# Optimization experiments

Hardware: AMD Instinct MI355X
Metric: run time of the kernel (lower is better)

The kernel has to match this reference:

```python
import jax, jax.numpy as jnp
import numpy as np

B, S, D = 4, 2048, 1024
H = 16
HD = D // H  # 64


def setup_inputs() -> dict:
    key = jax.random.key(0)
    ks = jax.random.split(key, 4)
    scale = 0.02
    return {
        "hidden_states": jax.random.normal(ks[0], (B, S, D), dtype=jnp.float32),
        "attention_mask": jnp.zeros((B, 1, 1, S), dtype=jnp.float32),
        "Wq": jax.random.normal(ks[1], (D, D), dtype=jnp.float32) * scale,
        "bq": jnp.zeros((D,), dtype=jnp.float32),
        "Wk": jax.random.normal(ks[2], (D, D), dtype=jnp.float32) * scale,
        "bk": jnp.zeros((D,), dtype=jnp.float32),
        "Wv": jax.random.normal(ks[3], (D, D), dtype=jnp.float32) * scale,
        "bv": jnp.zeros((D,), dtype=jnp.float32),
    }


def reference(hidden_states, attention_mask, Wq, bq, Wk, bk, Wv, bv):
    # linear projections: x @ W^T + b (torch nn.Linear convention); here W stored as [D,D]
    def proj(x, W, b):
        y = jnp.einsum("bsd,ed->bse", x, W) + b
        # [B,S,D] -> [B,H,S,HD]
        return y.reshape(B, S, H, HD).transpose(0, 2, 1, 3)

    q = proj(hidden_states, Wq, bq)
    k = proj(hidden_states, Wk, bk)
    v = proj(hidden_states, Wv, bv)

    scores = jnp.einsum("bhqd,bhkd->bhqk", q, k) / jnp.sqrt(jnp.float32(HD))
    scores = scores + attention_mask  # additive mask broadcast [B,1,1,S]
    probs = jax.nn.softmax(scores, axis=-1)  # dropout p=0 -> identity
    ctx = jnp.einsum("bhqk,bhkd->bhqd", probs, v)
    ctx = ctx.transpose(0, 2, 1, 3).reshape(B, S, D)
    return ctx
```

## Files before the change

### kernel.cpp

```cpp
#include <hip/hip_runtime.h>
#include <hip/hip_bf16.h>

typedef __attribute__((ext_vector_type(4))) float f32x4;
typedef __attribute__((ext_vector_type(16))) float f32x16;
typedef __attribute__((ext_vector_type(8))) short bf16x8;
typedef __attribute__((ext_vector_type(4))) unsigned int u32x4;
typedef unsigned short u16;

#define DEV static __device__ __forceinline__

DEV u16 f2bf(float f) {
    union { float f; unsigned int u; } v; v.f = f;
    unsigned int r = v.u + 0x7FFFu + ((v.u >> 16) & 1u);
    return (u16)(r >> 16);
}

DEV unsigned int cvt_pk(float lo, float hi) {
    unsigned int r;
    asm("v_cvt_pk_bf16_f32 %0, %1, %2" : "=v"(r) : "v"(lo), "v"(hi));
    return r;
}

DEV void pswap(unsigned int& a, unsigned int& b) {
    asm volatile("v_permlane32_swap_b32 %0, %1" : "+v"(a), "+v"(b));
}

DEV void async16(const void* g, void* l) {
    __builtin_amdgcn_global_load_lds((const __attribute__((address_space(1))) unsigned int*)g,
                                     (__attribute__((address_space(3))) unsigned int*)l, 16, 0, 0);
}

__global__ void cvt_all(const float4* __restrict__ x, const float4* __restrict__ wq,
                        const float4* __restrict__ wk, const float4* __restrict__ wv,
                        ushort4* __restrict__ xb, ushort4* __restrict__ wb,
                        const float* __restrict__ mask, float* __restrict__ em) {
    int bid = blockIdx.x;
    if (bid >= 11264) {
        int i = (bid - 11264) * 256 + threadIdx.x;
        em[i] = __builtin_amdgcn_exp2f(mask[i] * 1.44269504088896340736f);
        return;
    }
    const float4* s;
    ushort4* d;
    int i;
    if (bid < 8192) {
        s = x; d = xb; i = bid * 256 + threadIdx.x;
    } else {
        int r = bid - 8192;
        int wsel = r >> 10;
        s = (wsel == 0) ? wq : (wsel == 1) ? wk : wv;
        d = wb + (size_t)wsel * 262144;
        i = (r & 1023) * 256 + threadIdx.x;
    }
    float4 v = s[i];
    ushort4 o;
    o.x = f2bf(v.x); o.y = f2bf(v.y); o.z = f2bf(v.z); o.w = f2bf(v.w);
    d[i] = o;
}

__launch_bounds__(256, 2)
__global__ void qkv_gemm(const u16* __restrict__ xb, const u16* __restrict__ wb,
                         const float* __restrict__ bq, const float* __restrict__ bk,
                         const float* __restrict__ bv, const float* __restrict__ em,
                         u16* __restrict__ Qb, u16* __restrict__ Kb, u16* __restrict__ Vtb) {
    __shared__ u16 Al[2][128 * 64];
    __shared__ u16 Bl[2][128 * 64];
    const int t = threadIdx.x, ln = t & 63, w = t >> 6;
    const int wr = w >> 1, wc = w & 1;
    const int m0 = blockIdx.x * 128, e0 = blockIdx.y * 128, p = blockIdx.z;
    const u16* Wp = wb + (size_t)p * 1048576;
    const float* bias = (p == 0) ? bq : (p == 1) ? bk : bv;

    const int srow = t >> 3, scol = (t & 7) * 8;

    f32x4 acc[4][4];
#pragma unroll
    for (int i = 0; i < 4; i++)
#pragma unroll
        for (int j = 0; j < 4; j++) acc[i][j] = (f32x4){0.f, 0.f, 0.f, 0.f};

#define G_STAGE(buf, kk)                                                              \
    {                                                                                 \
        _Pragma("unroll")                                                             \
        for (int c = 0; c < 4; c++) {                                                 \
            int r = c * 32 + srow;                                                    \
            async16(&xb[(size_t)(m0 + r) * 1024 + (kk) + scol], &Al[buf][r * 64 + scol]); \
            async16(&Wp[(size_t)(e0 + r) * 1024 + (kk) + scol], &Bl[buf][r * 64 + scol]); \
        }                                                                             \
    }

    G_STAGE(0, 0);
    __syncthreads();
    int cur = 0;
    for (int kt = 0; kt < 16; kt++) {
        if (kt < 15) G_STAGE(cur ^ 1, (kt + 1) * 64);
#pragma unroll
        for (int kc = 0; kc < 2; kc++) {
            bf16x8 a[4], bb[4];
#pragma unroll
            for (int mf = 0; mf < 4; mf++)
                a[mf] = *(const bf16x8*)&Al[cur][(wr * 64 + mf * 16 + (ln & 15)) * 64 + kc * 32 + (ln >> 4) * 8];
#pragma unroll
            for (int nf = 0; nf < 4; nf++)
                bb[nf] = *(const bf16x8*)&Bl[cur][(wc * 64 + nf * 16 + (ln & 15)) * 64 + kc * 32 + (ln >> 4) * 8];
            __builtin_amdgcn_s_setprio(1);
#pragma unroll
            for (int mf = 0; mf < 4; mf++)
#pragma unroll
                for (int nf = 0; nf < 4; nf++)
                    acc[mf][nf] = __builtin_amdgcn_mfma_f32_16x16x32_bf16(a[mf], bb[nf], acc[mf][nf], 0, 0, 0);
            __builtin_amdgcn_s_setprio(0);
        }
        __syncthreads();
        cur ^= 1;
    }
#undef G_STAGE

    const int q16 = ln & 15, g = ln >> 4;
    if (p == 2) {
#pragma unroll
        for (int nf = 0; nf < 4; nf++) {
            int e = e0 + wc * 64 + nf * 16 + q16;
            float bias_v = bias[e];
            int h = e >> 6, hd = e & 63;
#pragma unroll
            for (int mf = 0; mf < 4; mf++) {
                int m = m0 + wr * 64 + mf * 16 + g * 4;
                int b = m >> 11, s = m & 2047;
                f32x4 emv = *(const f32x4*)&em[b * 2048 + s];
                ushort4 pk;
                pk.x = f2bf((acc[mf][nf][0] + bias_v) * emv[0]);
                pk.y = f2bf((acc[mf][nf][1] + bias_v) * emv[1]);
                pk.z = f2bf((acc[mf][nf][2] + bias_v) * emv[2]);
                pk.w = f2bf((acc[mf][nf][3] + bias_v) * emv[3]);
                *(ushort4*)&Vtb[((size_t)((b * 16 + h) * 64 + hd)) * 2048 + s] = pk;
            }
        }
    } else {
        const float qscale = (p == 0) ? 0.18033688011112042f : 1.0f;
        u16* out = (p == 0) ? Qb : Kb;
#pragma unroll
        for (int nf = 0; nf < 4; nf++) {
            int e = e0 + wc * 64 + nf * 16 + q16;
            float bias_v = bias[e];
            int h = e >> 6, hd = e & 63;
#pragma unroll
            for (int mf = 0; mf < 4; mf++) {
#pragma unroll
                for (int r = 0; r < 4; r++) {
                    int m = m0 + wr * 64 + mf * 16 + g * 4 + r;
                    int b = m >> 11, s = m & 2047;
                    out[((size_t)(b * 16 + h) * 2048 + s) * 64 + hd] = f2bf((acc[mf][nf][r] + bias_v) * qscale);
                }
            }
        }
    }
}

__launch_bounds__(128, 3)
__global__ void attn_kernel(const u16* __restrict__ Q, const u16* __restrict__ K,
                            const u16* __restrict__ Vt, const float* __restrict__ em,
                            float* __restrict__ out) {
    __shared__ u16 Kl[64 * 64];
    __shared__ u16 Vl[64 * 64];
    const int t = threadIdx.x, ln = t & 63, w = t >> 6;
    const int ln31 = ln & 31, hi = ln >> 5, ln7 = ln & 7;

    const int bid0 = blockIdx.x;
    const int swz = (bid0 & 7) * 256 + (bid0 >> 3);
    const int qbi = swz & 31, bh = swz >> 5;
    const int b = bh >> 4, h = bh & 15;
    const int qr = qbi * 64 + w * 32;
    const size_t base = (size_t)bh * 2048 * 64;

    bf16x8 aq[4];
#pragma unroll
    for (int ds = 0; ds < 4; ds++)
        aq[ds] = *(const bf16x8*)&Q[base + (size_t)(qr + ln31) * 64 + ds * 16 + hi * 8];

    const int rbase = t >> 3;
    const int sc = (t & 7) ^ (rbase & 7);

#define A_STAGE(kk)                                                                        \
    {                                                                                      \
        _Pragma("unroll")                                                                  \
        for (int i = 0; i < 4; i++) {                                                      \
            int row = i * 16 + rbase;                                                      \
            async16(&K[base + (size_t)((kk) + row) * 64 + sc * 8], &Kl[(i * 128 + t) * 8]); \
            async16(&Vt[base + (size_t)row * 2048 + (kk) + sc * 8], &Vl[(i * 128 + t) * 8]); \
        }                                                                                  \
    }

    f32x16 accT[2];
    accT[0] = (f32x16){};
    accT[1] = (f32x16){};
    f32x4 lacc = (f32x4){0.f, 0.f, 0.f, 0.f};

    for (int kt = 0; kt < 32; kt++) {
        const int k0 = kt * 64;
        if (kt) __syncthreads();
        A_STAGE(k0);
        __syncthreads();

#pragma unroll
        for (int kti = 0; kti < 2; kti++) {
            bf16x8 ka[4];
#pragma unroll
            for (int ds = 0; ds < 4; ds++)
                ka[ds] = *(const bf16x8*)&Kl[(kti * 32 + ln31) * 64 + (((ds << 1) | hi) ^ ln7) * 8];

            f32x4 em4[4];
#pragma unroll
            for (int rf = 0; rf < 4; rf++)
                em4[rf] = *(const f32x4*)&em[b * 2048 + k0 + kti * 32 + rf * 8 + hi * 4];

            f32x16 z = (f32x16){};
            __builtin_amdgcn_s_setprio(1);
#pragma unroll
            for (int ds = 0; ds < 4; ds++)
                z = __builtin_amdgcn_mfma_f32_32x32x16_bf16(ka[ds], aq[ds], z, 0, 0, 0);
            __builtin_amdgcn_s_setprio(0);

            float p[16];
#pragma unroll
            for (int i = 0; i < 16; i++) p[i] = __builtin_amdgcn_exp2f(z[i]);

#pragma unroll
            for (int rf = 0; rf < 4; rf++) {
                lacc[0] += p[4 * rf + 0] * em4[rf][0];
                lacc[1] += p[4 * rf + 1] * em4[rf][1];
                lacc[2] += p[4 * rf + 2] * em4[rf][2];
                lacc[3] += p[4 * rf + 3] * em4[rf][3];
            }

            unsigned int pk00 = cvt_pk(p[0], p[1]),   pk01 = cvt_pk(p[2], p[3]);
            unsigned int pk10 = cvt_pk(p[4], p[5]),   pk11 = cvt_pk(p[6], p[7]);
            unsigned int pk20 = cvt_pk(p[8], p[9]),   pk21 = cvt_pk(p[10], p[11]);
            unsigned int pk30 = cvt_pk(p[12], p[13]), pk31 = cvt_pk(p[14], p[15]);
            pswap(pk00, pk10); pswap(pk01, pk11);
            pswap(pk20, pk30); pswap(pk21, pk31);
            u32x4 pb[2];
            pb[0][0] = pk00; pb[0][1] = pk01; pb[0][2] = pk10; pb[0][3] = pk11;
            pb[1][0] = pk20; pb[1][1] = pk21; pb[1][2] = pk30; pb[1][3] = pk31;

            __builtin_amdgcn_s_setprio(1);
#pragma unroll
            for (int s = 0; s < 2; s++) {
                bf16x8 pv = *(const bf16x8*)&pb[s];
#pragma unroll
                for (int dt = 0; dt < 2; dt++) {
                    bf16x8 va = *(const bf16x8*)&Vl[(dt * 32 + ln31) * 64 +
                                                    ((kti * 4 + s * 2 + hi) ^ ln7) * 8];
                    accT[dt] = __builtin_amdgcn_mfma_f32_32x32x16_bf16(va, pv, accT[dt], 0, 0, 0);
                }
            }
            __builtin_amdgcn_s_setprio(0);
        }
    }
#undef A_STAGE

    float l = (lacc[0] + lacc[1]) + (lacc[2] + lacc[3]);
    l += __shfl_xor(l, 32);
    float inv = 1.0f / l;
    int q = qr + ln31;
#pragma unroll
    for (int dt = 0; dt < 2; dt++) {
#pragma unroll
        for (int rf = 0; rf < 4; rf++) {
            f32x4 o;
            o[0] = accT[dt][4 * rf + 0] * inv;
            o[1] = accT[dt][4 * rf + 1] * inv;
            o[2] = accT[dt][4 * rf + 2] * inv;
            o[3] = accT[dt][4 * rf + 3] * inv;
            *(f32x4*)&out[((size_t)(b * 2048 + q)) * 1024 + h * 64 + dt * 32 + rf * 8 + hi * 4] = o;
        }
    }
}

extern "C" void kernel_launch(void* const* d_in, const int* in_sizes, int n_in,
                              void* d_out, int out_size, void* d_ws, size_t ws_size,
                              hipStream_t stream) {
    const float* x    = (const float*)d_in[0];
    const float* mask = (const float*)d_in[1];
    const float* Wq   = (const float*)d_in[2];
    const float* bq   = (const float*)d_in[3];
    const float* Wk   = (const float*)d_in[4];
    const float* bk   = (const float*)d_in[5];
    const float* Wv   = (const float*)d_in[6];
    const float* bv   = (const float*)d_in[7];
    float* out = (float*)d_out;

    char* ws = (char*)d_ws;
    if (ws_size < (size_t)73433088) return;
    u16* xb   = (u16*)(ws);
    u16* wb   = (u16*)(ws + 16777216);
    u16* Qb   = (u16*)(ws + 23068672);
    u16* Kb   = (u16*)(ws + 39845888);
    u16* Vtb  = (u16*)(ws + 56623104);
    float* em = (float*)(ws + 73400320);

    cvt_all<<<11296, 256, 0, stream>>>((const float4*)x, (const float4*)Wq, (const float4*)Wk,
                                       (const float4*)Wv, (ushort4*)xb, (ushort4*)wb, mask, em);
    qkv_gemm<<<dim3(64, 8, 3), 256, 0, stream>>>(xb, wb, bq, bk, bv, em, Qb, Kb, Vtb);
    attn_kernel<<<2048, 128, 0, stream>>>(Qb, Kb, Vtb, em, out);
}
```

Baseline: 196.5 us.

## Double-buffer K/V tiles with 4-wave blocks and stage mask in LDS

The attention kernel moves from 2-wave blocks covering 64 query rows to 4-wave blocks covering 128 rows, so each K/V tile staged in shared memory serves twice as many waves. K/V staging is now double-buffered: the next tile is prefetched asynchronously while the current one is consumed, which removes one barrier per iteration and overlaps loads with MFMA work. The per-batch mask vector is copied once into LDS rather than read from global memory every step. The cost is more LDS per block (about 40KB), which may limit how many blocks fit per CU, and the grid halves to 1024 blocks.

After: 170.7 us. 13.2% less time.

```diff
diff --git a/kernel.cpp b/kernel.cpp
--- a/kernel.cpp
+++ b/kernel.cpp
@@ -157,20 +157,21 @@
     }
 }
 
-__launch_bounds__(128, 3)
+__launch_bounds__(256, 4)
 __global__ void attn_kernel(const u16* __restrict__ Q, const u16* __restrict__ K,
                             const u16* __restrict__ Vt, const float* __restrict__ em,
                             float* __restrict__ out) {
-    __shared__ u16 Kl[64 * 64];
-    __shared__ u16 Vl[64 * 64];
+    __shared__ u16 Kl[2][64 * 64];
+    __shared__ u16 Vl[2][64 * 64];
+    __shared__ float eml[2048];
     const int t = threadIdx.x, ln = t & 63, w = t >> 6;
     const int ln31 = ln & 31, hi = ln >> 5, ln7 = ln & 7;
 
     const int bid0 = blockIdx.x;
-    const int swz = (bid0 & 7) * 256 + (bid0 >> 3);
-    const int qbi = swz & 31, bh = swz >> 5;
+    const int swz = (bid0 & 7) * 128 + (bid0 >> 3);
+    const int qbi = swz & 15, bh = swz >> 4;
     const int b = bh >> 4, h = bh & 15;
-    const int qr = qbi * 64 + w * 32;
+    const int qr = qbi * 128 + w * 32;
     const size_t base = (size_t)bh * 2048 * 64;
 
     bf16x8 aq[4];
@@ -178,16 +179,25 @@
     for (int ds = 0; ds < 4; ds++)
         aq[ds] = *(const bf16x8*)&Q[base + (size_t)(qr + ln31) * 64 + ds * 16 + hi * 8];
 
-    const int rbase = t >> 3;
-    const int sc = (t & 7) ^ (rbase & 7);
-
-#define A_STAGE(kk)                                                                        \
+    {
+        const float4* src = (const float4*)&em[b * 2048];
+#pragma unroll
+        for (int i = 0; i < 2; i++) {
+            float4 v = src[i * 256 + t];
+            *(float4*)&eml[(i * 256 + t) * 4] = v;
+        }
+    }
+
+    const int rb = t >> 3;
+    const int sc = (t & 7) ^ (rb & 7);
+
+#define A_STAGE(buf, kk)                                                                   \
     {                                                                                      \
         _Pragma("unroll")                                                                  \
-        for (int i = 0; i < 4; i++) {                                                      \
-            int row = i * 16 + rbase;                                                      \
-            async16(&K[base + (size_t)((kk) + row) * 64 + sc * 8], &Kl[(i * 128 + t) * 8]); \
-            async16(&Vt[base + (size_t)row * 2048 + (kk) + sc * 8], &Vl[(i * 128 + t) * 8]); \
+        for (int i = 0; i < 2; i++) {                                                      \
+            int row = i * 32 + rb;                                                         \
+            async16(&K[base + (size_t)((kk) + row) * 64 + sc * 8], &Kl[buf][(i * 256 + t) * 8]); \
+            async16(&Vt[base + (size_t)row * 2048 + (kk) + sc * 8], &Vl[buf][(i * 256 + t) * 8]); \
         }                                                                                  \
     }
 
@@ -196,23 +206,25 @@
     accT[1] = (f32x16){};
     f32x4 lacc = (f32x4){0.f, 0.f, 0.f, 0.f};
 
+    A_STAGE(0, 0);
+    __syncthreads();
+    int cur = 0;
+
     for (int kt = 0; kt < 32; kt++) {
         const int k0 = kt * 64;
-        if (kt) __syncthreads();
-        A_STAGE(k0);
-        __syncthreads();
+        if (kt < 31) A_STAGE(cur ^ 1, k0 + 64);
 
 #pragma unroll
         for (int kti = 0; kti < 2; kti++) {
             bf16x8 ka[4];
 #pragma unroll
             for (int ds = 0; ds < 4; ds++)
-                ka[ds] = *(const bf16x8*)&Kl[(kti * 32 + ln31) * 64 + (((ds << 1) | hi) ^ ln7) * 8];
+                ka[ds] = *(const bf16x8*)&Kl[cur][(kti * 32 + ln31) * 64 + (((ds << 1) | hi) ^ ln7) * 8];
 
             f32x4 em4[4];
 #pragma unroll
             for (int rf = 0; rf < 4; rf++)
-                em4[rf] = *(const f32x4*)&em[b * 2048 + k0 + kti * 32 + rf * 8 + hi * 4];
+                em4[rf] = *(const f32x4*)&eml[k0 + kti * 32 + rf * 8 + hi * 4];
 
             f32x16 z = (f32x16){};
             __builtin_amdgcn_s_setprio(1);
@@ -249,13 +261,16 @@
                 bf16x8 pv = *(const bf16x8*)&pb[s];
 #pragma unroll
                 for (int dt = 0; dt < 2; dt++) {
-                    bf16x8 va = *(const bf16x8*)&Vl[(dt * 32 + ln31) * 64 +
-                                                    ((kti * 4 + s * 2 + hi) ^ ln7) * 8];
+                    bf16x8 va = *(const bf16x8*)&Vl[cur][(dt * 32 + ln31) * 64 +
+                                                         ((kti * 4 + s * 2 + hi) ^ ln7) * 8];
                     accT[dt] = __builtin_amdgcn_mfma_f32_32x32x16_bf16(va, pv, accT[dt], 0, 0, 0);
                 }
             }
             __builtin_amdgcn_s_setprio(0);
         }
+
+        __syncthreads();
+        cur ^= 1;
     }
 #undef A_STAGE
 
@@ -302,5 +317,5 @@
     cvt_all<<<11296, 256, 0, stream>>>((const float4*)x, (const float4*)Wq, (const float4*)Wk,
                                        (const float4*)Wv, (ushort4*)xb, (ushort4*)wb, mask, em);
     qkv_gemm<<<dim3(64, 8, 3), 256, 0, stream>>>(xb, wb, bq, bk, bv, em, Qb, Kb, Vtb);
-    attn_kernel<<<2048, 128, 0, stream>>>(Qb, Kb, Vtb, em, out);
-}
+    attn_kernel<<<1024, 256, 0, stream>>>(Qb, Kb, Vtb, em, out);
+}
```
